# Kernel optimization log

Hardware: AMD Instinct MI355X
Metric: run time of the kernel (lower is better)

The kernel has to match this reference:

```python
import jax, jax.numpy as jnp
import numpy as np

B, S, D, H, F = 4, 1024, 1024, 16, 4096
DH = D // H
EPS = 1e-5


def _ln(x, g, b):
    mu = jnp.mean(x, axis=-1, keepdims=True)
    var = jnp.mean((x - mu) ** 2, axis=-1, keepdims=True)
    return (x - mu) * jax.lax.rsqrt(var + EPS) * g + b


def _mha(q_in, k_in, v_in, mask, wq, bq, wk, bk, wv, bv, wo, bo):
    b, sq, d = q_in.shape
    sk = k_in.shape[1]
    Q = (q_in @ wq + bq).reshape(b, sq, H, DH).transpose(0, 2, 1, 3)  # [B,H,Sq,dh]
    K = (k_in @ wk + bk).reshape(b, sk, H, DH).transpose(0, 2, 1, 3)
    V = (v_in @ wv + bv).reshape(b, sk, H, DH).transpose(0, 2, 1, 3)
    scores = jnp.einsum('bhqd,bhkd->bhqk', Q, K) / jnp.sqrt(jnp.asarray(DH, Q.dtype))
    if mask is not None:
        scores = jnp.where(mask[:, None] == 0, jnp.asarray(-1e9, scores.dtype), scores)
    w = jax.nn.softmax(scores, axis=-1)
    ctx = jnp.einsum('bhqk,bhkd->bhqd', w, V).transpose(0, 2, 1, 3).reshape(b, sq, d)
    return ctx @ wo + bo


def setup_inputs() -> dict:
    key = jax.random.key(0)
    ks = jax.random.split(key, 20)
    s = 0.02
    inp = {
        'x': jax.random.normal(ks[0], (B, S, D), jnp.float32),
        'src_x': jax.random.normal(ks[1], (B, S, D), jnp.float32),
        # causal self-attention mask (1 = keep), cross mask all ones
        'mask': jnp.broadcast_to(jnp.tril(jnp.ones((S, S), jnp.int32)), (B, S, S)),
        'src_mask': jnp.ones((B, S, S), jnp.int32),
        'ln1_g': jnp.ones((D,), jnp.float32), 'ln1_b': jnp.zeros((D,), jnp.float32),
        'ln2_g': jnp.ones((D,), jnp.float32), 'ln2_b': jnp.zeros((D,), jnp.float32),
        'ln3_g': jnp.ones((D,), jnp.float32), 'ln3_b': jnp.zeros((D,), jnp.float32),
    }
    names = ['sa_wq', 'sa_wk', 'sa_wv', 'sa_wo', 'ca_wq', 'ca_wk', 'ca_wv', 'ca_wo']
    for i, n in enumerate(names):
        inp[n] = jax.random.normal(ks[2 + i], (D, D), jnp.float32) * s
        inp[n.replace('w', 'b')] = jnp.zeros((D,), jnp.float32)
    inp['ff_w1'] = jax.random.normal(ks[10], (D, F), jnp.float32) * s
    inp['ff_b1'] = jnp.zeros((F,), jnp.float32)
    inp['ff_w2'] = jax.random.normal(ks[11], (F, D), jnp.float32) * s
    inp['ff_b2'] = jnp.zeros((D,), jnp.float32)
    return inp


def reference(x, mask, src_x, src_mask,
              ln1_g, ln1_b, ln2_g, ln2_b, ln3_g, ln3_b,
              sa_wq, sa_bq, sa_wk, sa_bk, sa_wv, sa_bv, sa_wo, sa_bo,
              ca_wq, ca_bq, ca_wk, ca_bk, ca_wv, ca_bv, ca_wo, ca_bo,
              ff_w1, ff_b1, ff_w2, ff_b2):
    # pre-layer-norm decoder layer (dropout = 0 / eval mode)
    h = _ln(x, ln1_g, ln1_b)
    x = x + _mha(h, h, h, mask, sa_wq, sa_bq, sa_wk, sa_bk, sa_wv, sa_bv, sa_wo, sa_bo)
    h = _ln(x, ln2_g, ln2_b)
    x = x + _mha(h, src_x, src_x, src_mask, ca_wq, ca_bq, ca_wk, ca_bk, ca_wv, ca_bv, ca_wo, ca_bo)
    h = _ln(x, ln3_g, ln3_b)
    x = x + (jax.nn.relu(h @ ff_w1 + ff_b1) @ ff_w2 + ff_b2)
    return x
```

## Files before the change

kernel.cpp:

```cpp
#include <hip/hip_runtime.h>
#include <hip/hip_bf16.h>

#define B_ 4
#define S_ 1024
#define D_ 1024
#define H_ 16
#define DH_ 64
#define F_ 4096

typedef unsigned short u16;
typedef unsigned int u32;
typedef __attribute__((ext_vector_type(8))) short bf16x8;
typedef __attribute__((ext_vector_type(4))) short bf16x4;
typedef __attribute__((ext_vector_type(4))) float f32x4;

__device__ __forceinline__ float bf2f(u16 u) {
    return __uint_as_float(((u32)u) << 16);
}
__device__ __forceinline__ u16 f2bf(float f) {
    __hip_bfloat16 h = __float2bfloat16(f);
    return *reinterpret_cast<u16*>(&h);
}

typedef __attribute__((address_space(1))) const u32 gu32;
typedef __attribute__((address_space(3))) u32 lu32;
__device__ __forceinline__ void gl_lds16(const void* g, void* l) {
    __builtin_amdgcn_global_load_lds((gu32*)g, (lu32*)l, 16, 0, 0);
}

__device__ __forceinline__ void barrier_c() {
    asm volatile("" ::: "memory");
    __builtin_amdgcn_s_barrier();
    asm volatile("" ::: "memory");
}

__global__ __launch_bounds__(256) void cvt1_kernel(const float* __restrict__ s,
                                                   u16* __restrict__ d) {
    int i = (blockIdx.x * 256 + threadIdx.x) * 4;
    float4 v = *(const float4*)(s + i);
    u16 o0 = f2bf(v.x), o1 = f2bf(v.y), o2 = f2bf(v.z), o3 = f2bf(v.w);
    d[i] = o0; d[i+1] = o1; d[i+2] = o2; d[i+3] = o3;
}

__device__ __forceinline__ void trcvt_body(const float* __restrict__ src,
                                           u16* __restrict__ dst, int K, int N,
                                           int n0, int k0) {
    __shared__ u16 tile[64][65];
    int t = threadIdx.x;
    int c = t & 63, r4 = t >> 6;
#pragma unroll
    for (int i = 0; i < 16; i++) {
        int r = i * 4 + r4;
        tile[c][r] = f2bf(src[(size_t)(k0 + r) * N + n0 + c]);
    }
    __syncthreads();
#pragma unroll
    for (int i = 0; i < 16; i++) {
        int rr = i * 4 + r4;
        dst[(size_t)(n0 + rr) * K + k0 + c] = tile[rr][c];
    }
}

__global__ __launch_bounds__(256) void trcvt_kernel(const float* __restrict__ src,
                                                    u16* __restrict__ dst,
                                                    int K, int N) {
    trcvt_body(src, dst, K, N, blockIdx.x * 64, blockIdx.y * 64);
}

struct TP { const float* src[8]; u16* dst[8]; };
__global__ __launch_bounds__(256) void trcvt8_kernel(TP tp) {
    trcvt_body(tp.src[blockIdx.z], tp.dst[blockIdx.z], D_, D_,
               blockIdx.x * 64, blockIdx.y * 64);
}

__global__ __launch_bounds__(256) void mask_reduce_kernel(const int* __restrict__ mask,
                                                          unsigned char* __restrict__ bmask) {
    int t = threadIdx.x;
    int qb = blockIdx.x >> 4, kb = blockIdx.x & 15, b = blockIdx.y;
    bool all1 = true, any1 = false;
#pragma unroll
    for (int i = 0; i < 16; i++) {
        int e = t + i * 256;
        int r = e >> 6, c = e & 63;
        int v = mask[((size_t)(b * S_ + qb * 64 + r)) * S_ + kb * 64 + c];
        all1 = all1 && (v != 0);
        any1 = any1 || (v != 0);
    }
    unsigned long long ba = __ballot(all1), bn = __ballot(any1);
    __shared__ unsigned long long sa[4], sn[4];
    if ((t & 63) == 0) { sa[t >> 6] = ba; sn[t >> 6] = bn; }
    __syncthreads();
    if (t == 0) {
        bool A = ((sa[0] & sa[1] & sa[2] & sa[3]) == ~0ull);
        bool Y = ((sn[0] | sn[1] | sn[2] | sn[3]) != 0ull);
        bmask[b * 256 + blockIdx.x] = A ? 2 : (Y ? 1 : 0);
    }
}

template<bool COPY>
__global__ __launch_bounds__(256) void ln_kernel(const float* __restrict__ xin,
                                                 const float* __restrict__ g,
                                                 const float* __restrict__ bta,
                                                 float* xcur,
                                                 u16* __restrict__ hout) {
    int row = blockIdx.x;
    int t = threadIdx.x;
    size_t base = (size_t)row * D_;
    float v[4];
#pragma unroll
    for (int i = 0; i < 4; i++) v[i] = xin[base + t + i * 256];
    float s  = v[0] + v[1] + v[2] + v[3];
    float s2 = v[0]*v[0] + v[1]*v[1] + v[2]*v[2] + v[3]*v[3];
#pragma unroll
    for (int m = 1; m < 64; m <<= 1) {
        s  += __shfl_xor(s, m);
        s2 += __shfl_xor(s2, m);
    }
    __shared__ float red[8];
    int wave = t >> 6;
    if ((t & 63) == 0) { red[wave*2] = s; red[wave*2+1] = s2; }
    __syncthreads();
    float fs  = red[0] + red[2] + red[4] + red[6];
    float fs2 = red[1] + red[3] + red[5] + red[7];
    float mu  = fs * (1.0f / D_);
    float var = fs2 * (1.0f / D_) - mu * mu;
    float rs  = rsqrtf(var + 1e-5f);
#pragma unroll
    for (int i = 0; i < 4; i++) {
        int c = t + i * 256;
        float x = v[i];
        if (COPY) xcur[base + c] = x;
        hout[base + c] = f2bf((x - mu) * rs * g[c] + bta[c]);
    }
}

struct Bias3 { const float* b0; const float* b1; const float* b2; int n1; int n2; };

__device__ __forceinline__ float bias_at(const Bias3& bs, int c) {
    const float* p; int o;
    if (c < bs.n1)      { p = bs.b0; o = c; }
    else if (c < bs.n2) { p = bs.b1; o = c - bs.n1; }
    else                { p = bs.b2; o = c - bs.n2; }
    return p[o];
}

template<int BM, int BN, int OUT_MODE, bool BIAS_ROW>
__device__ __forceinline__ void gemm128_body(const u16* __restrict__ A,
                                             const u16* __restrict__ Bt,
                                             Bias3 bias,
                                             const float* res,
                                             void* out,
                                             int M, int N, int K,
                                             int lda, int ldb) {
    constexpr int MT = (BM == 64) ? 4 : (BN == 64 ? 2 : 4);
    constexpr int NT = (BN == 64) ? 4 : (BM == 64 ? 2 : 4);
    __shared__ u16 As[2][BM * 64];
    __shared__ u16 Bs[2][BN * 64];
    int t = threadIdx.x;
    int nx = gridDim.x;
    int nwg = nx * gridDim.y;
    int bid = blockIdx.y * nx + blockIdx.x;
    int swz = (bid & 7) * (nwg >> 3) + (bid >> 3);
    int m0 = (swz / nx) * BM, n0 = (swz % nx) * BN;
    int w = t >> 6, lane = t & 63, quad = lane >> 4, l16 = lane & 15;
    int wm, wn;
    if (BM == 128 && BN == 128) { wm = (w >> 1) * 64; wn = (w & 1) * 64; }
    else if (BN == 64)          { wm = w * 32;        wn = 0; }
    else                        { wm = 0;             wn = w * 32; }

    f32x4 acc[MT][NT] = {};
    int sr = lane >> 3;
    int gc = ((lane & 7) ^ sr) * 8;
    int x7 = l16 & 7;
    const u16* gA = A + (size_t)m0 * lda;
    const u16* gB = Bt + (size_t)n0 * ldb;

    auto stage = [&](int k0, int buf) {
#pragma unroll
        for (int j = w; j < BM / 8; j += 4)
            gl_lds16(gA + (size_t)(j * 8 + sr) * lda + k0 + gc, &As[buf][j * 512]);
#pragma unroll
        for (int j = w; j < BN / 8; j += 4)
            gl_lds16(gB + (size_t)(j * 8 + sr) * ldb + k0 + gc, &Bs[buf][j * 512]);
    };

    stage(0, 0);
    int cur = 0;
    for (int k0 = 0; k0 < K; k0 += 64) {
        __syncthreads();
        if (k0 + 64 < K) stage(k0 + 64, cur ^ 1);

#pragma unroll
        for (int s = 0; s < 2; s++) {
            bf16x8 af[MT], bfr[NT];
            int cp = ((s * 4 + quad) ^ x7) * 8;
#pragma unroll
            for (int mt = 0; mt < MT; mt++)
                af[mt] = *(const bf16x8*)&As[cur][(wm + mt * 16 + l16) * 64 + cp];
#pragma unroll
            for (int nt = 0; nt < NT; nt++)
                bfr[nt] = *(const bf16x8*)&Bs[cur][(wn + nt * 16 + l16) * 64 + cp];
#pragma unroll
            for (int mt = 0; mt < MT; mt++)
#pragma unroll
                for (int nt = 0; nt < NT; nt++)
                    acc[mt][nt] = __builtin_amdgcn_mfma_f32_16x16x32_bf16(af[mt], bfr[nt], acc[mt][nt], 0, 0, 0);
        }
        cur ^= 1;
    }

#pragma unroll
    for (int nt = 0; nt < NT; nt++) {
        int col = n0 + wn + nt * 16 + l16;
        float bc = (OUT_MODE == 3) ? 0.f : (BIAS_ROW ? 0.f : bias_at(bias, col));
#pragma unroll
        for (int mt = 0; mt < MT; mt++) {
#pragma unroll
            for (int r = 0; r < 4; r++) {
                int row = m0 + wm + mt * 16 + quad * 4 + r;
                float v = acc[mt][nt][r] + bc;
                if (OUT_MODE != 3 && BIAS_ROW) v += bias_at(bias, row);
                if (OUT_MODE == 1) v = fmaxf(v, 0.f);
                if (OUT_MODE == 2) {
                    v += res[(size_t)row * N + col];
                    ((float*)out)[(size_t)row * N + col] = v;
                } else if (OUT_MODE == 3) {
                    ((float*)out)[(size_t)row * N + col] = v;
                } else if (OUT_MODE == 4) {
                    int pc = (col & ~63) | (col & 32) | ((col & 0xC) << 1) |
                             ((col & 0x10) >> 2) | (col & 3);
                    ((u16*)out)[(size_t)row * N + pc] = f2bf(v);
                } else {
                    ((u16*)out)[(size_t)row * N + col] = f2bf(v);
                }
            }
        }
    }
}

template<int BM, int BN, int OUT_MODE, bool BIAS_ROW>
__global__ __launch_bounds__(256) void gemm128_kernel(const u16* __restrict__ A,
                                                      const u16* __restrict__ Bt,
                                                      Bias3 bias,
                                                      const float* res,
                                                      void* out,
                                                      int M, int N, int K) {
    gemm128_body<BM, BN, OUT_MODE, BIAS_ROW>(A, Bt, bias, res, out, M, N, K, K, K);
}

__global__ __launch_bounds__(256) void gemm128_splitk2_kernel(const u16* __restrict__ A,
                                                              const u16* __restrict__ Bt,
                                                              float* __restrict__ p0,
                                                              float* __restrict__ p1,
                                                              int M, int N, int Kh, int ld) {
    int z = blockIdx.z;
    Bias3 dummy = { nullptr, nullptr, nullptr, 1 << 30, 1 << 30 };
    gemm128_body<128, 128, 3, false>(A + z * Kh, Bt + z * Kh, dummy, nullptr,
                                     z ? (void*)p1 : (void*)p0, M, N, Kh, ld, ld);
}

__global__ __launch_bounds__(256) void ffn2_reduce_kernel(const float* __restrict__ p0,
                                                          const float* __restrict__ p1,
                                                          const float* __restrict__ b2,
                                                          const float* __restrict__ res,
                                                          float* __restrict__ out) {
    int i = (blockIdx.x * 256 + threadIdx.x) * 4;
    int col = i & (D_ - 1);
    float4 a = *(const float4*)(p0 + i);
    float4 b = *(const float4*)(p1 + i);
    float4 r = *(const float4*)(res + i);
    float4 bb = *(const float4*)(b2 + col);
    float4 o;
    o.x = a.x + b.x + r.x + bb.x;
    o.y = a.y + b.y + r.y + bb.y;
    o.z = a.z + b.z + r.z + bb.z;
    o.w = a.w + b.w + r.w + bb.w;
    *(float4*)(out + i) = o;
}

struct Pair2 {
    const u16* A0; const u16* A1;
    const u16* B0; const u16* B1;
    const float* b0; const float* b1;
    u16* o0; u16* o1;
};
__global__ __launch_bounds__(256) void gemm128_pairqk_kernel(Pair2 p, int M, int N, int K) {
    int z = blockIdx.z;
    const u16* A  = z ? p.A1 : p.A0;
    const u16* Bt = z ? p.B1 : p.B0;
    const float* bb = z ? p.b1 : p.b0;
    u16* o = z ? p.o1 : p.o0;
    Bias3 bs = { bb, bb, bb, 1 << 30, 1 << 30 };
    gemm128_body<128, 128, 0, false>(A, Bt, bs, nullptr, o, M, N, K, K, K);
}

__global__ __launch_bounds__(512) void gemm8p_kernel(const u16* __restrict__ A,
                                                     const u16* __restrict__ Bt,
                                                     const float* __restrict__ bias,
                                                     u16* __restrict__ out,
                                                     int M, int N, int K) {
    __shared__ u16 smem[65536];
    u16* Asb = smem;
    u16* Bsb = smem + 32768;
    int t = threadIdx.x;
    int w = t >> 6, lane = t & 63, quad = lane >> 4, l16 = lane & 15;
    int wr = w >> 2, wc = w & 3;
    int nx = gridDim.x;
    int nwg = nx * gridDim.y;
    int bid = blockIdx.y * nx + blockIdx.x;
    int swz = (bid & 7) * (nwg >> 3) + (bid >> 3);
    int n0 = (swz % nx) * 256, m0 = (swz / nx) * 256;
    int sr = lane >> 3, gc = ((lane & 7) ^ sr) * 8;
    const u16* gA = A + (size_t)m0 * K;
    const u16* gB = Bt + (size_t)n0 * K;

    f32x4 acc[8][4] = {};
    int ntt = K >> 6;

    auto stageA = [&](int ti) {
        int buf = ti & 1, k0 = ti << 6;
        gl_lds16(gA + (size_t)(w * 8 + sr) * K + k0 + gc,             Asb + buf * 16384 + w * 512);
        gl_lds16(gA + (size_t)((w + 8) * 8 + sr) * K + k0 + gc,       Asb + buf * 16384 + (w + 8) * 512);
        gl_lds16(gA + (size_t)(128 + w * 8 + sr) * K + k0 + gc,       Asb + buf * 16384 + 8192 + w * 512);
        gl_lds16(gA + (size_t)(128 + (w + 8) * 8 + sr) * K + k0 + gc, Asb + buf * 16384 + 8192 + (w + 8) * 512);
    };
    auto stageB = [&](int ti) {
        int buf = ti & 1, k0 = ti << 6;
        gl_lds16(gB + (size_t)(w * 8 + sr) * K + k0 + gc,             Bsb + buf * 16384 + w * 512);
        gl_lds16(gB + (size_t)((w + 8) * 8 + sr) * K + k0 + gc,       Bsb + buf * 16384 + (w + 8) * 512);
        gl_lds16(gB + (size_t)(128 + w * 8 + sr) * K + k0 + gc,       Bsb + buf * 16384 + 8192 + w * 512);
        gl_lds16(gB + (size_t)(128 + (w + 8) * 8 + sr) * K + k0 + gc, Bsb + buf * 16384 + 8192 + (w + 8) * 512);
    };

    stageA(0); stageB(0);
    stageA(1); stageB(1);

    for (int ti = 0; ti < ntt; ++ti) {
        int buf = ti & 1;
        if (ti == ntt - 1) asm volatile("s_waitcnt vmcnt(0)" ::: "memory");
        else               asm volatile("s_waitcnt vmcnt(8)" ::: "memory");
        __builtin_amdgcn_sched_barrier(0);
        barrier_c();
        const u16* Ah = Asb + buf * 16384 + wr * 8192;
        const u16* Bh = Bsb + buf * 16384 + (wc >> 1) * 8192;
        int br0 = (wc & 1) * 64;
        bf16x8 a0[8], a1[8], b0[4], b1[4];

#pragma unroll
        for (int mt = 0; mt < 8; mt++) {
            int lr = mt * 16 + l16;
            a0[mt] = *(const bf16x8*)&Ah[lr * 64 + ((quad ^ (lr & 7)) * 8)];
        }
#pragma unroll
        for (int nt = 0; nt < 4; nt++) {
            int lr = br0 + nt * 16 + l16;
            b0[nt] = *(const bf16x8*)&Bh[lr * 64 + ((quad ^ (lr & 7)) * 8)];
        }
        __builtin_amdgcn_s_setprio(1);
#pragma unroll
        for (int mt = 0; mt < 4; mt++)
#pragma unroll
            for (int nt = 0; nt < 4; nt++)
                acc[mt][nt] = __builtin_amdgcn_mfma_f32_16x16x32_bf16(a0[mt], b0[nt], acc[mt][nt], 0, 0, 0);
        __builtin_amdgcn_s_setprio(0);
        barrier_c();

#pragma unroll
        for (int mt = 0; mt < 8; mt++) {
            int lr = mt * 16 + l16;
            a1[mt] = *(const bf16x8*)&Ah[lr * 64 + (((4 + quad) ^ (lr & 7)) * 8)];
        }
        __builtin_amdgcn_s_setprio(1);
#pragma unroll
        for (int mt = 4; mt < 8; mt++)
#pragma unroll
            for (int nt = 0; nt < 4; nt++)
                acc[mt][nt] = __builtin_amdgcn_mfma_f32_16x16x32_bf16(a0[mt], b0[nt], acc[mt][nt], 0, 0, 0);
        __builtin_amdgcn_s_setprio(0);
        asm volatile("s_waitcnt lgkmcnt(0)" ::: "memory");
        __builtin_amdgcn_sched_barrier(0);
        barrier_c();

#pragma unroll
        for (int nt = 0; nt < 4; nt++) {
            int lr = br0 + nt * 16 + l16;
            b1[nt] = *(const bf16x8*)&Bh[lr * 64 + (((4 + quad) ^ (lr & 7)) * 8)];
        }
        if (ti + 2 < ntt) stageA(ti + 2);
        __builtin_amdgcn_s_setprio(1);
#pragma unroll
        for (int mt = 0; mt < 4; mt++)
#pragma unroll
            for (int nt = 0; nt < 4; nt++)
                acc[mt][nt] = __builtin_amdgcn_mfma_f32_16x16x32_bf16(a1[mt], b1[nt], acc[mt][nt], 0, 0, 0);
        __builtin_amdgcn_s_setprio(0);
        asm volatile("s_waitcnt lgkmcnt(0)" ::: "memory");
        __builtin_amdgcn_sched_barrier(0);
        barrier_c();

        if (ti + 2 < ntt) stageB(ti + 2);
        __builtin_amdgcn_s_setprio(1);
#pragma unroll
        for (int mt = 4; mt < 8; mt++)
#pragma unroll
            for (int nt = 0; nt < 4; nt++)
                acc[mt][nt] = __builtin_amdgcn_mfma_f32_16x16x32_bf16(a1[mt], b1[nt], acc[mt][nt], 0, 0, 0);
        __builtin_amdgcn_s_setprio(0);
    }

    barrier_c();
    u16* ot = smem;
#pragma unroll
    for (int nt = 0; nt < 4; nt++) {
        float bc = bias[n0 + wc * 64 + nt * 16 + l16];
        int csw = wc * 64 + ((nt ^ quad) * 16) + l16;
#pragma unroll
        for (int mt = 0; mt < 8; mt++) {
#pragma unroll
            for (int r = 0; r < 4; r++) {
                int row = wr * 128 + mt * 16 + quad * 4 + r;
                ot[row * 256 + csw] = f2bf(fmaxf(acc[mt][nt][r] + bc, 0.f));
            }
        }
    }
    barrier_c();
    int tr = t >> 5, tc = t & 31;
#pragma unroll
    for (int ps = 0; ps < 16; ps++) {
        int row = ps * 16 + tr;
        int qd = (row >> 2) & 3;
        int csw = (tc * 8) ^ (qd << 4);
        bf16x8 v = *(const bf16x8*)&ot[row * 256 + csw];
        *(bf16x8*)&out[(size_t)(m0 + row) * N + n0 + tc * 8] = v;
    }
}

__global__ __launch_bounds__(256) void attn_kernel(const u16* __restrict__ Q, int ldq,
                                                   const u16* __restrict__ Kb, int ldk,
                                                   const u16* __restrict__ Vt,
                                                   const int* __restrict__ mask,
                                                   const unsigned char* __restrict__ bmask,
                                                   u16* __restrict__ ctx) {
    __shared__ u16 Ks[2][64 * 64];
    __shared__ u16 Vs[2][64 * 64];
    int t = threadIdx.x;
    int b = blockIdx.z, hh = blockIdx.y, qt = blockIdx.x;
    int w = t >> 6, lane = t & 63, quad = lane >> 4, l16 = lane & 15;
    int hoff = hh * DH_;

    bf16x8 ones8;
#pragma unroll
    for (int j = 0; j < 8; j++) ones8[j] = (short)0x3F80;

    bf16x8 qf[2];
    int qrow = qt * 64 + w * 16 + l16;
#pragma unroll
    for (int kk = 0; kk < 2; kk++) {
        bf16x8 v = *(const bf16x8*)(Q + (size_t)(b * S_ + qrow) * ldq + hoff + kk * 32 + quad * 8);
#pragma unroll
        for (int j = 0; j < 8; j++)
            v[j] = (short)f2bf(bf2f((u16)v[j]) * 0.125f);
        qf[kk] = v;
    }

    f32x4 oacc[4] = {};
    f32x4 lacc = {};

    unsigned nz = 0, mx = 0;
    for (int c = 0; c < 16; c++) {
        int v = bmask ? (int)bmask[(b * 16 + qt) * 16 + c] : 1;
        if (v)      nz |= 1u << c;
        if (v == 1) mx |= 1u << c;
    }

    int sr = lane >> 3;
    int gc = ((lane & 7) ^ sr) * 8;

    auto stage64 = [&](int c, int buf) {
        int k0 = c * 64;
        for (int j = w; j < 8; j += 4) {
            gl_lds16(Kb + (size_t)(b * S_ + k0 + j * 8 + sr) * ldk + hoff + gc, &Ks[buf][j * 512]);
            gl_lds16(Vt + (size_t)(hoff + j * 8 + sr) * (B_ * S_) + b * S_ + k0 + gc, &Vs[buf][j * 512]);
        }
    };

    unsigned rem = nz;
    int c = rem ? __builtin_ctz(rem) : -1;
    if (c >= 0) stage64(c, 0);
    int cur = 0;

    while (c >= 0) {
        rem &= rem - 1;
        int nc = rem ? __builtin_ctz(rem) : -1;
        __syncthreads();
        if (nc >= 0) stage64(nc, cur ^ 1);

        int k0c = c * 64;
        bool mixed = (mx >> c) & 1u;
        const u16* KsT = Ks[cur];
        const u16* VsT = Vs[cur];

        float p[4][4];
#pragma unroll
        for (int nt = 0; nt < 4; nt++) {
            f32x4 sacc = {};
            int krow = nt * 16 + l16;
            __builtin_amdgcn_s_setprio(1);
#pragma unroll
            for (int kk = 0; kk < 2; kk++) {
                int cp = ((kk * 4 + quad) ^ (krow & 7)) * 8;
                bf16x8 kf = *(const bf16x8*)&KsT[krow * 64 + cp];
                sacc = __builtin_amdgcn_mfma_f32_16x16x32_bf16(kf, qf[kk], sacc, 0, 0, 0);
            }
            __builtin_amdgcn_s_setprio(0);
#pragma unroll
            for (int r = 0; r < 4; r++) {
                float sv = sacc[r];
                if (mixed) {
                    int kc = k0c + nt * 16 + quad * 4 + r;
                    if (mask[(size_t)(b * S_ + qrow) * S_ + kc] == 0) sv = -1e9f;
                }
                p[nt][r] = __expf(fminf(sv, 20.f));
            }
        }

#pragma unroll
        for (int mp = 0; mp < 2; mp++) {
            bf16x8 af;
#pragma unroll
            for (int r = 0; r < 4; r++) {
                af[r]     = (short)f2bf(p[2 * mp][r]);
                af[4 + r] = (short)f2bf(p[2 * mp + 1][r]);
            }
            __builtin_amdgcn_s_setprio(1);
            lacc = __builtin_amdgcn_mfma_f32_16x16x32_bf16(af, ones8, lacc, 0, 0, 0);
#pragma unroll
            for (int dt = 0; dt < 4; dt++) {
                int vrow = dt * 16 + l16;
                int ch = (mp * 4 + quad) ^ (vrow & 7);
                bf16x8 vf = *(const bf16x8*)&VsT[vrow * 64 + ch * 8];
                oacc[dt] = __builtin_amdgcn_mfma_f32_16x16x32_bf16(af, vf, oacc[dt], 0, 0, 0);
            }
            __builtin_amdgcn_s_setprio(0);
        }
        c = nc;
        cur ^= 1;
    }

#pragma unroll
    for (int dt = 0; dt < 4; dt++)
#pragma unroll
        for (int r = 0; r < 4; r++) {
            int qq = qt * 64 + w * 16 + quad * 4 + r;
            float l = lacc[r];
            float inv = l > 0.f ? 1.f / l : 0.f;
            ctx[(size_t)(b * S_ + qq) * D_ + hoff + dt * 16 + l16] = f2bf(oacc[dt][r] * inv);
        }
}

extern "C" void kernel_launch(void* const* d_in, const int* in_sizes, int n_in,
                              void* d_out, int out_size, void* d_ws, size_t ws_size,
                              hipStream_t stream) {
    const float* x     = (const float*)d_in[0];
    const float* srcx  = (const float*)d_in[1];
    const int*   mask  = (const int*)d_in[2];
    const int*   smask = (const int*)d_in[3];
    const float* ln1g = (const float*)d_in[4],  *ln1b = (const float*)d_in[5];
    const float* ln2g = (const float*)d_in[6],  *ln2b = (const float*)d_in[7];
    const float* ln3g = (const float*)d_in[8],  *ln3b = (const float*)d_in[9];
    const float* sa_wq = (const float*)d_in[10], *sa_bq = (const float*)d_in[11];
    const float* sa_wk = (const float*)d_in[12], *sa_bk = (const float*)d_in[13];
    const float* sa_wv = (const float*)d_in[14], *sa_bv = (const float*)d_in[15];
    const float* sa_wo = (const float*)d_in[16], *sa_bo = (const float*)d_in[17];
    const float* ca_wq = (const float*)d_in[18], *ca_bq = (const float*)d_in[19];
    const float* ca_wk = (const float*)d_in[20], *ca_bk = (const float*)d_in[21];
    const float* ca_wv = (const float*)d_in[22], *ca_bv = (const float*)d_in[23];
    const float* ca_wo = (const float*)d_in[24], *ca_bo = (const float*)d_in[25];
    const float* ff_w1 = (const float*)d_in[26], *ff_b1 = (const float*)d_in[27];
    const float* ff_w2 = (const float*)d_in[28], *ff_b2 = (const float*)d_in[29];

    char* ws = (char*)d_ws;
    const size_t MB = 1ull << 20;
    const size_t DD = (size_t)D_ * D_;
    float* xcur = (float*)ws;
    u16* h     = (u16*)(ws + 16 * MB);
    u16* qk    = (u16*)(ws + 24 * MB);
    u16* qb    = (u16*)(ws + 24 * MB);
    u16* kbuf  = (u16*)(ws + 32 * MB);
    u16* vt    = (u16*)(ws + 40 * MB);
    u16* ctx   = (u16*)(ws + 48 * MB);
    u16* ff    = (u16*)(ws + 24 * MB);
    u16* sxb   = (u16*)(ws + 56 * MB);
    u16* wqk_s = (u16*)(ws + 64 * MB);
    u16* wv_s  = (u16*)(ws + 68 * MB);
    u16* wo_s  = (u16*)(ws + 70 * MB);
    u16* wq_c  = (u16*)(ws + 72 * MB);
    u16* wk_c  = (u16*)(ws + 74 * MB);
    u16* wv_c  = (u16*)(ws + 76 * MB);
    u16* wo_c  = (u16*)(ws + 78 * MB);
    u16* wff1  = (u16*)(ws + 80 * MB);
    u16* wff2  = (u16*)(ws + 88 * MB);
    float* fp0 = (float*)(ws + 56 * MB);
    float* fp1 = (float*)(ws + 72 * MB);
    unsigned char* bm_self = nullptr, *bm_cross = nullptr;
    if (ws_size >= 96 * MB + 8192) {
        bm_self  = (unsigned char*)(ws + ws_size - 8192);
        bm_cross = bm_self + 4096;
    }

    dim3 blk(256);

    TP tp = {{sa_wq, sa_wk, sa_wv, sa_wo, ca_wq, ca_wk, ca_wv, ca_wo},
             {wqk_s, wqk_s + DD, wv_s, wo_s, wq_c, wk_c, wv_c, wo_c}};
    trcvt8_kernel<<<dim3(16, 16, 8), blk, 0, stream>>>(tp);
    trcvt_kernel<<<dim3(F_ / 64, D_ / 64), blk, 0, stream>>>(ff_w1, wff1, D_, F_);
    trcvt_kernel<<<dim3(D_ / 64, F_ / 64), blk, 0, stream>>>(ff_w2, wff2, F_, D_);
    cvt1_kernel<<<B_ * S_ * D_ / 1024, blk, 0, stream>>>(srcx, sxb);
    if (bm_self) {
        mask_reduce_kernel<<<dim3(256, B_), blk, 0, stream>>>(mask, bm_self);
        mask_reduce_kernel<<<dim3(256, B_), blk, 0, stream>>>(smask, bm_cross);
    }

    Bias3 bqk = { sa_bq, sa_bk, sa_bk, 1024, 2048 };
    Bias3 bsv = { sa_bv, sa_bv, sa_bv, 1 << 30, 1 << 30 };
    Bias3 bso = { sa_bo, sa_bo, sa_bo, 1 << 30, 1 << 30 };
    Bias3 bcv = { ca_bv, ca_bv, ca_bv, 1 << 30, 1 << 30 };
    Bias3 bco = { ca_bo, ca_bo, ca_bo, 1 << 30, 1 << 30 };

    ln_kernel<true><<<B_ * S_, blk, 0, stream>>>(x, ln1g, ln1b, xcur, h);
    gemm128_kernel<128,128,0,false><<<dim3(16, 32), blk, 0, stream>>>(h, wqk_s, bqk, nullptr, qk, 4096, 2048, 1024);
    gemm128_kernel<64,128,4,true><<<dim3(32, 16), blk, 0, stream>>>(wv_s, h, bsv, nullptr, vt, 1024, 4096, 1024);
    attn_kernel<<<dim3(16, H_, B_), blk, 0, stream>>>(qk, 2048, qk + 1024, 2048, vt, mask, bm_self, ctx);
    gemm128_kernel<128,64,2,false><<<dim3(16, 32), blk, 0, stream>>>(ctx, wo_s, bso, xcur, xcur, 4096, 1024, 1024);

    ln_kernel<false><<<B_ * S_, blk, 0, stream>>>(xcur, ln2g, ln2b, nullptr, h);
    {
        Pair2 pqk = { h, sxb, wq_c, wk_c, ca_bq, ca_bk, qb, kbuf };
        gemm128_pairqk_kernel<<<dim3(8, 32, 2), blk, 0, stream>>>(pqk, 4096, 1024, 1024);
    }
    gemm128_kernel<64,128,4,true><<<dim3(32, 16), blk, 0, stream>>>(wv_c, sxb, bcv, nullptr, vt, 1024, 4096, 1024);
    attn_kernel<<<dim3(16, H_, B_), blk, 0, stream>>>(qb, 1024, kbuf, 1024, vt, smask, bm_cross, ctx);
    gemm128_kernel<128,64,2,false><<<dim3(16, 32), blk, 0, stream>>>(ctx, wo_c, bco, xcur, xcur, 4096, 1024, 1024);

    ln_kernel<false><<<B_ * S_, blk, 0, stream>>>(xcur, ln3g, ln3b, nullptr, h);
    gemm8p_kernel<<<dim3(16, 16), dim3(512), 0, stream>>>(h, wff1, ff_b1, ff, 4096, 4096, 1024);
    gemm128_splitk2_kernel<<<dim3(8, 32, 2), blk, 0, stream>>>(ff, wff2, fp0, fp1, 4096, 1024, 2048, 4096);
    ffn2_reduce_kernel<<<dim3(B_ * S_ * D_ / 1024), blk, 0, stream>>>(fp0, fp1, ff_b2, xcur, (float*)d_out);
}
```

Before: 530.3 us.

## Use 8-wave 256x128 pipelined split-K GEMM for FFN down-projection

Replaces the 128x128 split-K GEMM for the FFN second projection with a 512-thread kernel using 256x128 tiles. It double-buffers global-to-LDS loads, interleaves the staging with MFMA phases, and raises wave priority around the MFMA blocks. The larger tile raises operand reuse per LDS load. The cost is half as many workgroups (256 total) and more registers per thread.

```diff
diff --git a/kernel.cpp b/kernel.cpp
--- a/kernel.cpp
+++ b/kernel.cpp
@@ -248,17 +248,6 @@
     gemm128_body<BM, BN, OUT_MODE, BIAS_ROW>(A, Bt, bias, res, out, M, N, K, K, K);
 }
 
-__global__ __launch_bounds__(256) void gemm128_splitk2_kernel(const u16* __restrict__ A,
-                                                              const u16* __restrict__ Bt,
-                                                              float* __restrict__ p0,
-                                                              float* __restrict__ p1,
-                                                              int M, int N, int Kh, int ld) {
-    int z = blockIdx.z;
-    Bias3 dummy = { nullptr, nullptr, nullptr, 1 << 30, 1 << 30 };
-    gemm128_body<128, 128, 3, false>(A + z * Kh, Bt + z * Kh, dummy, nullptr,
-                                     z ? (void*)p1 : (void*)p0, M, N, Kh, ld, ld);
-}
-
 __global__ __launch_bounds__(256) void ffn2_reduce_kernel(const float* __restrict__ p0,
                                                           const float* __restrict__ p1,
                                                           const float* __restrict__ b2,
@@ -432,6 +421,132 @@
         int csw = (tc * 8) ^ (qd << 4);
         bf16x8 v = *(const bf16x8*)&ot[row * 256 + csw];
         *(bf16x8*)&out[(size_t)(m0 + row) * N + n0 + tc * 8] = v;
+    }
+}
+
+__global__ __launch_bounds__(512) void gemm8ps_kernel(const u16* __restrict__ A,
+                                                      const u16* __restrict__ Bt,
+                                                      float* __restrict__ p0,
+                                                      float* __restrict__ p1,
+                                                      int M, int N, int Kh, int ld) {
+    __shared__ u16 Asb[2 * 2 * 128 * 64];
+    __shared__ u16 Bsb[2 * 128 * 64];
+    int t = threadIdx.x;
+    int w = t >> 6, lane = t & 63, quad = lane >> 4, l16 = lane & 15;
+    int wr = w >> 2, wc = w & 3;
+    int z = blockIdx.z;
+    int nx = gridDim.x;
+    int nwg = nx * gridDim.y;
+    int bid = blockIdx.y * nx + blockIdx.x;
+    int swz = (bid & 7) * (nwg >> 3) + (bid >> 3);
+    int n0 = (swz % nx) * 128, m0 = (swz / nx) * 256;
+    int sr = lane >> 3, gc = ((lane & 7) ^ sr) * 8;
+    const u16* gA = A + (size_t)m0 * ld + z * Kh;
+    const u16* gB = Bt + (size_t)n0 * ld + z * Kh;
+    float* out = z ? p1 : p0;
+
+    f32x4 acc[8][2] = {};
+    int ntt = Kh >> 6;
+
+    auto stageA = [&](int ti) {
+        int buf = ti & 1, k0 = ti << 6;
+        gl_lds16(gA + (size_t)(w * 8 + sr) * ld + k0 + gc,             Asb + buf * 16384 + w * 512);
+        gl_lds16(gA + (size_t)((w + 8) * 8 + sr) * ld + k0 + gc,       Asb + buf * 16384 + (w + 8) * 512);
+        gl_lds16(gA + (size_t)(128 + w * 8 + sr) * ld + k0 + gc,       Asb + buf * 16384 + 8192 + w * 512);
+        gl_lds16(gA + (size_t)(128 + (w + 8) * 8 + sr) * ld + k0 + gc, Asb + buf * 16384 + 8192 + (w + 8) * 512);
+    };
+    auto stageB = [&](int ti) {
+        int buf = ti & 1, k0 = ti << 6;
+        gl_lds16(gB + (size_t)(w * 8 + sr) * ld + k0 + gc,       Bsb + buf * 8192 + w * 512);
+        gl_lds16(gB + (size_t)((w + 8) * 8 + sr) * ld + k0 + gc, Bsb + buf * 8192 + (w + 8) * 512);
+    };
+
+    stageA(0); stageB(0);
+    stageA(1); stageB(1);
+
+    for (int ti = 0; ti < ntt; ++ti) {
+        int buf = ti & 1;
+        if (ti == ntt - 1) asm volatile("s_waitcnt vmcnt(0)" ::: "memory");
+        else               asm volatile("s_waitcnt vmcnt(6)" ::: "memory");
+        __builtin_amdgcn_sched_barrier(0);
+        barrier_c();
+        const u16* Ah = Asb + buf * 16384 + wr * 8192;
+        const u16* Bh = Bsb + buf * 8192;
+        bf16x8 a0[8], a1[8], b0[2], b1[2];
+
+#pragma unroll
+        for (int mt = 0; mt < 8; mt++) {
+            int lr = mt * 16 + l16;
+            a0[mt] = *(const bf16x8*)&Ah[lr * 64 + ((quad ^ (lr & 7)) * 8)];
+        }
+#pragma unroll
+        for (int nt = 0; nt < 2; nt++) {
+            int lr = wc * 32 + nt * 16 + l16;
+            b0[nt] = *(const bf16x8*)&Bh[lr * 64 + ((quad ^ (lr & 7)) * 8)];
+        }
+        __builtin_amdgcn_s_setprio(1);
+#pragma unroll
+        for (int mt = 0; mt < 4; mt++)
+#pragma unroll
+            for (int nt = 0; nt < 2; nt++)
+                acc[mt][nt] = __builtin_amdgcn_mfma_f32_16x16x32_bf16(a0[mt], b0[nt], acc[mt][nt], 0, 0, 0);
+        __builtin_amdgcn_s_setprio(0);
+        barrier_c();
+
+#pragma unroll
+        for (int mt = 0; mt < 8; mt++) {
+            int lr = mt * 16 + l16;
+            a1[mt] = *(const bf16x8*)&Ah[lr * 64 + (((4 + quad) ^ (lr & 7)) * 8)];
+        }
+        __builtin_amdgcn_s_setprio(1);
+#pragma unroll
+        for (int mt = 4; mt < 8; mt++)
+#pragma unroll
+            for (int nt = 0; nt < 2; nt++)
+                acc[mt][nt] = __builtin_amdgcn_mfma_f32_16x16x32_bf16(a0[mt], b0[nt], acc[mt][nt], 0, 0, 0);
+        __builtin_amdgcn_s_setprio(0);
+        asm volatile("s_waitcnt lgkmcnt(0)" ::: "memory");
+        __builtin_amdgcn_sched_barrier(0);
+        barrier_c();
+
+#pragma unroll
+        for (int nt = 0; nt < 2; nt++) {
+            int lr = wc * 32 + nt * 16 + l16;
+            b1[nt] = *(const bf16x8*)&Bh[lr * 64 + (((4 + quad) ^ (lr & 7)) * 8)];
+        }
+        if (ti + 2 < ntt) stageA(ti + 2);
+        __builtin_amdgcn_s_setprio(1);
+#pragma unroll
+        for (int mt = 0; mt < 4; mt++)
+#pragma unroll
+            for (int nt = 0; nt < 2; nt++)
+                acc[mt][nt] = __builtin_amdgcn_mfma_f32_16x16x32_bf16(a1[mt], b1[nt], acc[mt][nt], 0, 0, 0);
+        __builtin_amdgcn_s_setprio(0);
+        asm volatile("s_waitcnt lgkmcnt(0)" ::: "memory");
+        __builtin_amdgcn_sched_barrier(0);
+        barrier_c();
+
+        if (ti + 2 < ntt) stageB(ti + 2);
+        __builtin_amdgcn_s_setprio(1);
+#pragma unroll
+        for (int mt = 4; mt < 8; mt++)
+#pragma unroll
+            for (int nt = 0; nt < 2; nt++)
+                acc[mt][nt] = __builtin_amdgcn_mfma_f32_16x16x32_bf16(a1[mt], b1[nt], acc[mt][nt], 0, 0, 0);
+        __builtin_amdgcn_s_setprio(0);
+    }
+
+#pragma unroll
+    for (int nt = 0; nt < 2; nt++) {
+        int col = n0 + wc * 32 + nt * 16 + l16;
+#pragma unroll
+        for (int mt = 0; mt < 8; mt++) {
+#pragma unroll
+            for (int r = 0; r < 4; r++) {
+                int row = m0 + wr * 128 + mt * 16 + quad * 4 + r;
+                out[(size_t)row * N + col] = acc[mt][nt][r];
+            }
+        }
     }
 }
 
@@ -644,6 +759,6 @@
 
     ln_kernel<false><<<B_ * S_, blk, 0, stream>>>(xcur, ln3g, ln3b, nullptr, h);
     gemm8p_kernel<<<dim3(16, 16), dim3(512), 0, stream>>>(h, wff1, ff_b1, ff, 4096, 4096, 1024);
-    gemm128_splitk2_kernel<<<dim3(8, 32, 2), blk, 0, stream>>>(ff, wff2, fp0, fp1, 4096, 1024, 2048, 4096);
+    gemm8ps_kernel<<<dim3(8, 16, 2), dim3(512), 0, stream>>>(ff, wff2, fp0, fp1, 4096, 1024, 2048, 4096);
     ffn2_reduce_kernel<<<dim3(B_ * S_ * D_ / 1024), blk, 0, stream>>>(fp0, fp1, ff_b2, xcur, (float*)d_out);
 }
```

Result: no change. 531.4 us (+0.2%).
